# Kernel tuning notes

Hardware: AMD Instinct MI355X
Metric: run time of the kernel (lower is better)

The kernel has to match this reference:

```python
import jax, jax.numpy as jnp
import numpy as np

STEPS = 8
TOL = 1e-6


def _kabsch(p, q):
    # p, q: [B, N, 3]; returns R [B,3,3], t [B,3] s.t. q ~= R p + t (pypose svdtf)
    pm = p.mean(axis=-2, keepdims=True)
    qm = q.mean(axis=-2, keepdims=True)
    pc = p - pm
    qc = q - qm
    H = jnp.einsum('bni,bnj->bij', pc, qc)          # 3x3 cross-covariance
    U, S, Vt = jnp.linalg.svd(H, full_matrices=False)
    V = jnp.swapaxes(Vt, -1, -2)
    Ut = jnp.swapaxes(U, -1, -2)
    d = jnp.linalg.det(jnp.matmul(V, Ut))            # reflection fix
    D = jnp.concatenate([jnp.ones(d.shape + (2,), d.dtype), d[..., None]], axis=-1)
    R = jnp.matmul(V * D[..., None, :], Ut)
    t = qm[..., 0, :] - jnp.einsum('bij,bj->bi', R, pm[..., 0, :])
    return R, t


def _rotmat_to_quat(R):
    # branchless rotation-matrix -> quaternion [qx, qy, qz, qw] (pypose order)
    r00, r11, r22 = R[..., 0, 0], R[..., 1, 1], R[..., 2, 2]
    qw = 0.5 * jnp.sqrt(jnp.clip(1.0 + r00 + r11 + r22, 1e-12))
    qx = 0.5 * jnp.sqrt(jnp.clip(1.0 + r00 - r11 - r22, 1e-12))
    qy = 0.5 * jnp.sqrt(jnp.clip(1.0 - r00 + r11 - r22, 1e-12))
    qz = 0.5 * jnp.sqrt(jnp.clip(1.0 - r00 - r11 + r22, 1e-12))
    qx = qx * jnp.where(R[..., 2, 1] - R[..., 1, 2] >= 0, 1.0, -1.0)
    qy = qy * jnp.where(R[..., 0, 2] - R[..., 2, 0] >= 0, 1.0, -1.0)
    qz = qz * jnp.where(R[..., 1, 0] - R[..., 0, 1] >= 0, 1.0, -1.0)
    return jnp.stack([qx, qy, qz, qw], axis=-1)


def _icp(psrc, ptgt):
    B = psrc.shape[0]
    tn = (ptgt * ptgt).sum(-1)                        # [B, M]

    def body(carry, _):
        pc, err, done = carry
        # brute-force 1-NN: Euclidean cdist via  |p|^2 + |q|^2 - 2 p.q
        sq = ((pc * pc).sum(-1)[:, :, None] + tn[:, None, :]
              - 2.0 * jnp.einsum('bnd,bmd->bnm', pc, ptgt))
        dist = jnp.sqrt(jnp.clip(sq, 0.0))            # [B, N, M]
        knnd = dist.min(axis=-1)                      # [B, N]
        idx = dist.argmin(axis=-1)                    # [B, N]
        errnew = knnd.mean(axis=-1)                   # [B]
        conv = jnp.all(jnp.abs(errnew - err) < TOL)
        done_new = jnp.logical_or(done, conv)
        qk = jnp.take_along_axis(ptgt, jnp.broadcast_to(idx[..., None], pc.shape), axis=1)
        R, t = _kabsch(pc, qk)
        pcnew = jnp.einsum('bij,bnj->bni', R, pc) + t[:, None, :]
        pc = jnp.where(done_new, pc, pcnew)
        err = jnp.where(done_new, err, errnew)
        return (pc, err, done_new), None

    init = (psrc, jnp.zeros((B,), psrc.dtype), jnp.array(False))
    (pc, _, _), _ = jax.lax.scan(body, init, None, length=STEPS)
    R, t = _kabsch(psrc, pc)                          # final fit psrc -> moved cloud
    quat = _rotmat_to_quat(R)
    return jnp.concatenate([t, quat], axis=-1)        # SE3 7-vector [t, qx,qy,qz,qw]


def setup_inputs() -> dict:
    key = jax.random.key(0)
    k1, k2 = jax.random.split(key)
    psrc = jax.random.normal(k1, (2, 4096, 3), dtype=jnp.float32)
    ptgt = jax.random.normal(k2, (2, 4096, 3), dtype=jnp.float32)
    return {"psrc": psrc, "ptgt": ptgt}


def reference(psrc, ptgt):
    return _icp(psrc, ptgt)
```

## Files before the change

### kernel.cpp

```cpp
#include <hip/hip_runtime.h>
#include <math.h>

#define NPTS 4096
#define MPTS 4096
#define NSTEPS 8
#define ICP_TOL 1e-6f
#define NBLK 512
#define NSUB 32

#define ACC_OFF 32768
#define CTR_OFF 98304
#define CTR_STRIDE 1536
#define STPUB_OFF 110592

__global__ void init_kernel(const float* __restrict__ ptgt, float* __restrict__ ws) {
    float* ptgt4 = ws;
    unsigned* ctrs = (unsigned*)(ws + CTR_OFF);
    int gid = blockIdx.x * 256 + threadIdx.x;
    if (gid < 2 * MPTS) {
        float x = ptgt[3 * gid + 0];
        float y = ptgt[3 * gid + 1];
        float z = ptgt[3 * gid + 2];
        float4 v;
        v.x = x; v.y = y; v.z = z;
        v.w = 0.5f * (x * x + y * y + z * z);
        ((float4*)ptgt4)[gid] = v;
    }
    for (int i = gid; i < NSTEPS * CTR_STRIDE; i += 8192) ctrs[i] = 0u;
}

__device__ __forceinline__ float frcp(float x) {
#if __has_builtin(__builtin_amdgcn_rcpf)
    return __builtin_amdgcn_rcpf(x);
#else
    return 1.f / x;
#endif
}
__device__ __forceinline__ float frsq(float x) {
#if __has_builtin(__builtin_amdgcn_rsqf)
    return __builtin_amdgcn_rsqf(x);
#else
    return 1.f / sqrtf(x);
#endif
}

#define DET3(a,b,c,d,e,f,g,h,i) \
    ((a)*((e)*(i)-(f)*(h)) - (b)*((d)*(i)-(f)*(g)) + (c)*((d)*(h)-(e)*(g)))

__device__ __forceinline__ void horn_quat(const float N[4][4], float q[4]) {
    float s = 1e-30f;
#pragma unroll
    for (int i = 0; i < 4; ++i)
#pragma unroll
        for (int j = 0; j < 4; ++j) s = fmaxf(s, fabsf(N[i][j]));
    float inv = frcp(s);
    float A[4][4], B[4][4];
#pragma unroll
    for (int i = 0; i < 4; ++i)
#pragma unroll
        for (int j = 0; j < 4; ++j) A[i][j] = N[i][j] * inv;
#pragma unroll
    for (int i = 0; i < 4; ++i)
#pragma unroll
        for (int j = i; j < 4; ++j) {
            float v = A[i][0]*A[0][j] + A[i][1]*A[1][j] + A[i][2]*A[2][j] + A[i][3]*A[3][j];
            B[i][j] = v; B[j][i] = v;
        }
    float p1 = A[0][0]+A[1][1]+A[2][2]+A[3][3];
    float p2 = B[0][0]+B[1][1]+B[2][2]+B[3][3];
    float p3 = 0.f, p4 = 0.f;
#pragma unroll
    for (int i = 0; i < 4; ++i)
#pragma unroll
        for (int j = 0; j < 4; ++j) { p3 += A[i][j]*B[i][j]; p4 += B[i][j]*B[i][j]; }
    float e1 = p1;
    float e2 = 0.5f*(e1*p1 - p2);
    float e3 = (e2*p1 - e1*p2 + p3)*(1.f/3.f);
    float e4 = 0.25f*(e3*p1 - e2*p2 + e1*p3 - p4);
    float lam = -3e38f;
#pragma unroll
    for (int i = 0; i < 4; ++i) {
        float r = A[i][i];
#pragma unroll
        for (int j = 0; j < 4; ++j) if (j != i) r += fabsf(A[i][j]);
        lam = fmaxf(lam, r);
    }
#pragma unroll
    for (int it = 0; it < 12; ++it) {
        float pv = (((lam - e1)*lam + e2)*lam - e3)*lam + e4;
        float dv = ((4.f*lam - 3.f*e1)*lam + 2.f*e2)*lam - e3;
        lam -= pv * frcp(dv);
    }
    float M[4][4];
#pragma unroll
    for (int i = 0; i < 4; ++i)
#pragma unroll
        for (int j = 0; j < 4; ++j) M[i][j] = A[i][j] - ((i == j) ? lam : 0.f);
    float C0 = DET3(M[1][1],M[1][2],M[1][3], M[2][1],M[2][2],M[2][3], M[3][1],M[3][2],M[3][3]);
    float C1 = DET3(M[0][0],M[0][2],M[0][3], M[2][0],M[2][2],M[2][3], M[3][0],M[3][2],M[3][3]);
    float C2 = DET3(M[0][0],M[0][1],M[0][3], M[1][0],M[1][1],M[1][3], M[3][0],M[3][1],M[3][3]);
    float C3 = DET3(M[0][0],M[0][1],M[0][2], M[1][0],M[1][1],M[1][2], M[2][0],M[2][1],M[2][2]);
    int is = 0; float cb = fabsf(C0);
    if (fabsf(C1) > cb) { cb = fabsf(C1); is = 1; }
    if (fabsf(C2) > cb) { cb = fabsf(C2); is = 2; }
    if (fabsf(C3) > cb) { cb = fabsf(C3); is = 3; }
    float v0, v1, v2, v3;
#define ROWCOF(a,b,c) { \
    v0 =  DET3(M[a][1],M[a][2],M[a][3], M[b][1],M[b][2],M[b][3], M[c][1],M[c][2],M[c][3]); \
    v1 = -DET3(M[a][0],M[a][2],M[a][3], M[b][0],M[b][2],M[b][3], M[c][0],M[c][2],M[c][3]); \
    v2 =  DET3(M[a][0],M[a][1],M[a][3], M[b][0],M[b][1],M[b][3], M[c][0],M[c][1],M[c][3]); \
    v3 = -DET3(M[a][0],M[a][1],M[a][2], M[b][0],M[b][1],M[b][2], M[c][0],M[c][1],M[c][2]); }
    if (is == 0)      ROWCOF(1,2,3)
    else if (is == 1) ROWCOF(0,2,3)
    else if (is == 2) ROWCOF(0,1,3)
    else              ROWCOF(0,1,2)
#undef ROWCOF
    float nr = frsq(v0*v0 + v1*v1 + v2*v2 + v3*v3);
    q[0] = v0*nr; q[1] = v1*nr; q[2] = v2*nr; q[3] = v3*nr;
}

#define FOR16(OP) OP(0) OP(1) OP(2) OP(3) OP(4) OP(5) OP(6) OP(7) \
                  OP(8) OP(9) OP(10) OP(11) OP(12) OP(13) OP(14) OP(15)

__global__ __launch_bounds__(256, 2) void icp_main(
    const float* __restrict__ psrc, float* __restrict__ ws,
    float* __restrict__ out) {

    float* ptgt4 = ws;
    float* acc = ws + ACC_OFF;
    unsigned* ctrs = (unsigned*)(ws + CTR_OFF);
    float* stpub = ws + STPUB_OFF;

    __shared__ float st[2][13];
    __shared__ unsigned keys[4][16];
    __shared__ float red[16][16];
    __shared__ float gred[16][16];
    __shared__ float asum[2][16];
    __shared__ int contflag;

    const int tid = threadIdx.x;
    const int bid = blockIdx.x;
    const int b = bid >> 8;
    const int n0 = (bid & 255) * 16;

    if (tid < 2) {
        st[tid][0] = 1.f; st[tid][1] = 0.f; st[tid][2] = 0.f;
        st[tid][3] = 0.f; st[tid][4] = 1.f; st[tid][5] = 0.f;
        st[tid][6] = 0.f; st[tid][7] = 0.f; st[tid][8] = 1.f;
        st[tid][9] = 0.f; st[tid][10] = 0.f; st[tid][11] = 0.f;
        st[tid][12] = 0.f;
    }
    __syncthreads();

    const int w = tid >> 6, lane = tid & 63;
    const int m0 = w * 1024 + lane;
    const float4* tpb = (const float4*)ptgt4 + ((size_t)b * MPTS + m0);
    const float* ps = psrc + ((size_t)b * NPTS + n0) * 3;

    for (int step = 0; step < NSTEPS; ++step) {
        float R00 = st[b][0], R01 = st[b][1], R02 = st[b][2];
        float R10 = st[b][3], R11 = st[b][4], R12 = st[b][5];
        float R20 = st[b][6], R21 = st[b][7], R22 = st[b][8];
        float t0 = st[b][9], t1 = st[b][10], t2 = st[b][11];

#define DECLP(i) float px##i, py##i, pz##i;
        FOR16(DECLP)
#undef DECLP
#define LOADP(i) { float x = ps[3*(i)], y = ps[3*(i)+1], z = ps[3*(i)+2]; \
        px##i = fmaf(R00, x, fmaf(R01, y, fmaf(R02, z, t0))); \
        py##i = fmaf(R10, x, fmaf(R11, y, fmaf(R12, z, t1))); \
        pz##i = fmaf(R20, x, fmaf(R21, y, fmaf(R22, z, t2))); }
        FOR16(LOADP)
#undef LOADP

#define DECLB(i) float bs##i = -3.0e38f; int ix##i = m0;
        FOR16(DECLB)
#undef DECLB

        float4 tc0 = tpb[0];
        float4 tc1 = tpb[64];
        int mreg = m0;
#pragma unroll
        for (int k = 0; k < 16; ++k) {
            float4 tnx = tpb[((k + 2) & 15) * 64];
            float tx = tc0.x, ty = tc0.y, tz = tc0.z, htn = tc0.w;
#define PAIR(i) { float s = fmaf(px##i, tx, fmaf(py##i, ty, fmaf(pz##i, tz, -htn))); \
            if (s > bs##i) { bs##i = s; ix##i = mreg; } }
            FOR16(PAIR)
#undef PAIR
            mreg += 64;
            tc0 = tc1;
            tc1 = tnx;
        }

#define REDKEY(i) { unsigned ub = __float_as_uint(bs##i); \
        unsigned u = ((int)ub >= 0) ? (ub | 0x80000000u) : ~ub; \
        unsigned key = (u & 0xFFFFF000u) | (4095u - (unsigned)ix##i); \
        for (int off = 32; off; off >>= 1) { \
            unsigned o = (unsigned)__shfl_xor((int)key, off); \
            key = key > o ? key : o; } \
        if (lane == 0) keys[w][i] = key; }
        FOR16(REDKEY)
#undef REDKEY
        __syncthreads();

        if (tid < 16) {
            unsigned key = keys[0][tid];
            unsigned k1 = keys[1][tid], k2 = keys[2][tid], k3 = keys[3][tid];
            key = key > k1 ? key : k1;
            key = key > k2 ? key : k2;
            key = key > k3 ? key : k3;
            int m = 4095 - (int)(key & 0xFFFu);
            float4 qq = ((const float4*)ptgt4)[(size_t)b * MPTS + m];
            const float* pp = psrc + ((size_t)b * NPTS + n0 + tid) * 3;
            float x = pp[0], y = pp[1], z = pp[2];
            float px = fmaf(R00, x, fmaf(R01, y, fmaf(R02, z, t0)));
            float py = fmaf(R10, x, fmaf(R11, y, fmaf(R12, z, t1)));
            float pz = fmaf(R20, x, fmaf(R21, y, fmaf(R22, z, t2)));
            float dx = px - qq.x, dy = py - qq.y, dz = pz - qq.z;
            float dist = sqrtf(dx * dx + dy * dy + dz * dz);
            red[tid][0] = px; red[tid][1] = py; red[tid][2] = pz;
            red[tid][3] = qq.x; red[tid][4] = qq.y; red[tid][5] = qq.z;
            red[tid][6] = px * qq.x;  red[tid][7] = px * qq.y;  red[tid][8] = px * qq.z;
            red[tid][9] = py * qq.x;  red[tid][10] = py * qq.y; red[tid][11] = py * qq.z;
            red[tid][12] = pz * qq.x; red[tid][13] = pz * qq.y; red[tid][14] = pz * qq.z;
            red[tid][15] = dist;
        }
        __syncthreads();
        if (tid < 16) {
            float s = 0.f;
#pragma unroll
            for (int r = 0; r < 16; ++r) s += red[r][tid];
            __hip_atomic_store(&acc[((size_t)step * NBLK + bid) * 16 + tid], s,
                               __ATOMIC_RELAXED, __HIP_MEMORY_SCOPE_AGENT);
        }

        unsigned* stepc = ctrs + step * CTR_STRIDE;
        __syncthreads();
        if (tid == 0) {
            unsigned* sub = stepc + (bid & (NSUB - 1)) * 16;
            unsigned old = __hip_atomic_fetch_add(sub, 1u, __ATOMIC_RELAXED,
                                                  __HIP_MEMORY_SCOPE_AGENT);
            if (old == (unsigned)(NBLK / NSUB) - 1u)
                __hip_atomic_fetch_add(stepc + 512, 1u, __ATOMIC_RELAXED,
                                       __HIP_MEMORY_SCOPE_AGENT);
        }

        if (bid == 0) {
            if (tid == 0) {
                while (__hip_atomic_load(stepc + 512, __ATOMIC_RELAXED,
                                         __HIP_MEMORY_SCOPE_AGENT) < (unsigned)NSUB) {
                    __builtin_amdgcn_s_sleep(1);
                }
            }
            __syncthreads();
            {
                const float* accs = acc + (size_t)step * NBLK * 16;
                int c = tid & 15, g = tid >> 4;
                float ssum = 0.f;
#pragma unroll
                for (int i = 0; i < 32; ++i)
                    ssum += accs[(size_t)(g * 32 + i) * 16 + c];
                gred[g][c] = ssum;
            }
            __syncthreads();
            if (tid < 32) {
                int bb = tid >> 4, c = tid & 15;
                float s = 0.f;
#pragma unroll
                for (int g = 0; g < 8; ++g) s += gred[bb * 8 + g][c];
                asum[bb][c] = s;
            }
            __syncthreads();
            if (tid == 0) {
                float err0 = asum[0][15] * (1.f / NPTS);
                float err1 = asum[1][15] * (1.f / NPTS);
                bool conv = (fabsf(err0 - st[0][12]) < ICP_TOL) &&
                            (fabsf(err1 - st[1][12]) < ICP_TOL);
                contflag = conv ? 2 : 1;
            }
            __syncthreads();
            if (contflag == 1 && tid < 2) {
                float a[16];
                for (int i = 0; i < 16; ++i) a[i] = asum[tid][i];
                const float inv_n = 1.f / NPTS;
                float pmx = a[0]*inv_n, pmy = a[1]*inv_n, pmz = a[2]*inv_n;
                float qmx = a[3]*inv_n, qmy = a[4]*inv_n, qmz = a[5]*inv_n;
                float H[3][3];
                for (int i = 0; i < 3; ++i)
                    for (int j = 0; j < 3; ++j)
                        H[i][j] = a[6 + 3*i + j] - a[i]*a[3 + j]*inv_n;
                float Sxx=H[0][0], Sxy=H[0][1], Sxz=H[0][2];
                float Syx=H[1][0], Syy=H[1][1], Syz=H[1][2];
                float Szx=H[2][0], Szy=H[2][1], Szz=H[2][2];
                float Nm[4][4];
                Nm[0][0] = Sxx+Syy+Szz; Nm[0][1] = Syz-Szy;
                Nm[0][2] = Szx-Sxz;     Nm[0][3] = Sxy-Syx;
                Nm[1][1] = Sxx-Syy-Szz; Nm[1][2] = Sxy+Syx; Nm[1][3] = Szx+Sxz;
                Nm[2][2] = -Sxx+Syy-Szz; Nm[2][3] = Syz+Szy;
                Nm[3][3] = -Sxx-Syy+Szz;
                Nm[1][0]=Nm[0][1]; Nm[2][0]=Nm[0][2]; Nm[3][0]=Nm[0][3];
                Nm[2][1]=Nm[1][2]; Nm[3][1]=Nm[1][3]; Nm[3][2]=Nm[2][3];
                float qv[4];
                horn_quat(Nm, qv);
                float qw = qv[0], qx = qv[1], qy = qv[2], qz = qv[3];
                float R00n = 1.f - 2.f*(qy*qy + qz*qz);
                float R01n = 2.f*(qx*qy - qw*qz);
                float R02n = 2.f*(qx*qz + qw*qy);
                float R10n = 2.f*(qx*qy + qw*qz);
                float R11n = 1.f - 2.f*(qx*qx + qz*qz);
                float R12n = 2.f*(qy*qz - qw*qx);
                float R20n = 2.f*(qx*qz - qw*qy);
                float R21n = 2.f*(qy*qz + qw*qx);
                float R22n = 1.f - 2.f*(qx*qx + qy*qy);
                float tx = qmx - (R00n*pmx + R01n*pmy + R02n*pmz);
                float ty = qmy - (R10n*pmx + R11n*pmy + R12n*pmz);
                float tz = qmz - (R20n*pmx + R21n*pmy + R22n*pmz);
                float C00=st[tid][0], C01=st[tid][1], C02=st[tid][2];
                float C10=st[tid][3], C11=st[tid][4], C12=st[tid][5];
                float C20=st[tid][6], C21=st[tid][7], C22=st[tid][8];
                float T0=st[tid][9], T1=st[tid][10], T2=st[tid][11];
                float ns[12];
                ns[0] = R00n*C00 + R01n*C10 + R02n*C20;
                ns[1] = R00n*C01 + R01n*C11 + R02n*C21;
                ns[2] = R00n*C02 + R01n*C12 + R02n*C22;
                ns[3] = R10n*C00 + R11n*C10 + R12n*C20;
                ns[4] = R10n*C01 + R11n*C11 + R12n*C21;
                ns[5] = R10n*C02 + R11n*C12 + R12n*C22;
                ns[6] = R20n*C00 + R21n*C10 + R22n*C20;
                ns[7] = R20n*C01 + R21n*C11 + R22n*C21;
                ns[8] = R20n*C02 + R21n*C12 + R22n*C22;
                ns[9]  = R00n*T0 + R01n*T1 + R02n*T2 + tx;
                ns[10] = R10n*T0 + R11n*T1 + R12n*T2 + ty;
                ns[11] = R20n*T0 + R21n*T1 + R22n*T2 + tz;
                for (int i = 0; i < 12; ++i) {
                    st[tid][i] = ns[i];
                    __hip_atomic_store(&stpub[step*32 + tid*16 + i], ns[i],
                                       __ATOMIC_RELAXED, __HIP_MEMORY_SCOPE_AGENT);
                }
                st[tid][12] = asum[tid][15] * (1.f / NPTS);
            }
            __syncthreads();
            if (tid == 0) {
                unsigned fv = (unsigned)contflag;
#pragma unroll
                for (int f = 0; f < 32; ++f)
                    __hip_atomic_store(stepc + 1024 + f*16, fv,
                                       __ATOMIC_RELAXED, __HIP_MEMORY_SCOPE_AGENT);
            }
            __syncthreads();
        } else {
            if (tid == 0) {
                unsigned* myflag = stepc + 1024 + (bid & 31) * 16;
                unsigned fv;
                while ((fv = __hip_atomic_load(myflag, __ATOMIC_RELAXED,
                                               __HIP_MEMORY_SCOPE_AGENT)) == 0u) {
                    __builtin_amdgcn_s_sleep(2);
                }
                contflag = (int)fv;
                if (fv == 1u) {
                    for (int i = 0; i < 12; ++i)
                        st[b][i] = __hip_atomic_load(&stpub[step*32 + b*16 + i],
                                                     __ATOMIC_RELAXED,
                                                     __HIP_MEMORY_SCOPE_AGENT);
                }
            }
            __syncthreads();
        }
        if (contflag == 2) break;
    }

    if (bid == 0 && tid < 2) {
        float r00 = st[tid][0], r01 = st[tid][1], r02 = st[tid][2];
        float r10 = st[tid][3], r11 = st[tid][4], r12 = st[tid][5];
        float r20 = st[tid][6], r21 = st[tid][7], r22 = st[tid][8];
        float qw = 0.5f * sqrtf(fmaxf(1.f + r00 + r11 + r22, 1e-12f));
        float qx = 0.5f * sqrtf(fmaxf(1.f + r00 - r11 - r22, 1e-12f));
        float qy = 0.5f * sqrtf(fmaxf(1.f - r00 + r11 - r22, 1e-12f));
        float qz = 0.5f * sqrtf(fmaxf(1.f - r00 - r11 + r22, 1e-12f));
        qx = (r21 - r12 >= 0.f) ? qx : -qx;
        qy = (r02 - r20 >= 0.f) ? qy : -qy;
        qz = (r10 - r01 >= 0.f) ? qz : -qz;
        out[tid * 7 + 0] = st[tid][9];
        out[tid * 7 + 1] = st[tid][10];
        out[tid * 7 + 2] = st[tid][11];
        out[tid * 7 + 3] = qx;
        out[tid * 7 + 4] = qy;
        out[tid * 7 + 5] = qz;
        out[tid * 7 + 6] = qw;
    }
}

extern "C" void kernel_launch(void* const* d_in, const int* in_sizes, int n_in,
                              void* d_out, int out_size, void* d_ws, size_t ws_size,
                              hipStream_t stream) {
    const float* psrc = (const float*)d_in[0];
    const float* ptgt = (const float*)d_in[1];
    float* out = (float*)d_out;
    float* ws = (float*)d_ws;

    init_kernel<<<32, 256, 0, stream>>>(ptgt, ws);
    icp_main<<<NBLK, 256, 0, stream>>>(psrc, ws, out);
}
```

Before: 174.0 us.

## Replace master-block reduce-and-broadcast with redundant per-block reduction after grid barrier

Previously block 0 waited for all blocks, reduced the partial sums, ran the Horn solve and published the new transform, while every other block spun waiting for it. Now the last block to arrive at the hierarchical counter sets the release flags, and every block then reads all partial sums itself and runs the same reduction and solve locally. This removes one serialized publish-and-wait round trip per step, leaving a single barrier. The cost is 512 blocks each reading the full accumulator array (about 32 KB per step) and repeating the small solve, and all blocks must compute identical results for the convergence decision to stay consistent.

```diff
diff --git a/kernel.cpp b/kernel.cpp
--- a/kernel.cpp
+++ b/kernel.cpp
@@ -11,7 +11,6 @@
 #define ACC_OFF 32768
 #define CTR_OFF 98304
 #define CTR_STRIDE 1536
-#define STPUB_OFF 110592
 
 __global__ void init_kernel(const float* __restrict__ ptgt, float* __restrict__ ws) {
     float* ptgt4 = ws;
@@ -129,7 +128,6 @@
     float* ptgt4 = ws;
     float* acc = ws + ACC_OFF;
     unsigned* ctrs = (unsigned*)(ws + CTR_OFF);
-    float* stpub = ws + STPUB_OFF;
 
     __shared__ float st[2][13];
     __shared__ unsigned keys[4][16];
@@ -239,134 +237,114 @@
         __syncthreads();
         if (tid == 0) {
             unsigned* sub = stepc + (bid & (NSUB - 1)) * 16;
+            bool bcast = false;
             unsigned old = __hip_atomic_fetch_add(sub, 1u, __ATOMIC_RELAXED,
                                                   __HIP_MEMORY_SCOPE_AGENT);
-            if (old == (unsigned)(NBLK / NSUB) - 1u)
-                __hip_atomic_fetch_add(stepc + 512, 1u, __ATOMIC_RELAXED,
-                                       __HIP_MEMORY_SCOPE_AGENT);
-        }
-
-        if (bid == 0) {
-            if (tid == 0) {
-                while (__hip_atomic_load(stepc + 512, __ATOMIC_RELAXED,
-                                         __HIP_MEMORY_SCOPE_AGENT) < (unsigned)NSUB) {
+            if (old == (unsigned)(NBLK / NSUB) - 1u) {
+                unsigned mold = __hip_atomic_fetch_add(stepc + 512, 1u,
+                                    __ATOMIC_RELAXED, __HIP_MEMORY_SCOPE_AGENT);
+                if (mold == (unsigned)NSUB - 1u) {
+#pragma unroll
+                    for (int f = 0; f < NSUB; ++f)
+                        __hip_atomic_store(stepc + 1024 + f * 16, 1u,
+                                           __ATOMIC_RELAXED,
+                                           __HIP_MEMORY_SCOPE_AGENT);
+                    bcast = true;
+                }
+            }
+            if (!bcast) {
+                unsigned* myflag = stepc + 1024 + (bid & (NSUB - 1)) * 16;
+                while (__hip_atomic_load(myflag, __ATOMIC_RELAXED,
+                                         __HIP_MEMORY_SCOPE_AGENT) == 0u) {
                     __builtin_amdgcn_s_sleep(1);
                 }
             }
-            __syncthreads();
-            {
-                const float* accs = acc + (size_t)step * NBLK * 16;
-                int c = tid & 15, g = tid >> 4;
-                float ssum = 0.f;
-#pragma unroll
-                for (int i = 0; i < 32; ++i)
-                    ssum += accs[(size_t)(g * 32 + i) * 16 + c];
-                gred[g][c] = ssum;
-            }
-            __syncthreads();
-            if (tid < 32) {
-                int bb = tid >> 4, c = tid & 15;
-                float s = 0.f;
-#pragma unroll
-                for (int g = 0; g < 8; ++g) s += gred[bb * 8 + g][c];
-                asum[bb][c] = s;
-            }
-            __syncthreads();
-            if (tid == 0) {
-                float err0 = asum[0][15] * (1.f / NPTS);
-                float err1 = asum[1][15] * (1.f / NPTS);
-                bool conv = (fabsf(err0 - st[0][12]) < ICP_TOL) &&
-                            (fabsf(err1 - st[1][12]) < ICP_TOL);
-                contflag = conv ? 2 : 1;
-            }
-            __syncthreads();
-            if (contflag == 1 && tid < 2) {
-                float a[16];
-                for (int i = 0; i < 16; ++i) a[i] = asum[tid][i];
-                const float inv_n = 1.f / NPTS;
-                float pmx = a[0]*inv_n, pmy = a[1]*inv_n, pmz = a[2]*inv_n;
-                float qmx = a[3]*inv_n, qmy = a[4]*inv_n, qmz = a[5]*inv_n;
-                float H[3][3];
-                for (int i = 0; i < 3; ++i)
-                    for (int j = 0; j < 3; ++j)
-                        H[i][j] = a[6 + 3*i + j] - a[i]*a[3 + j]*inv_n;
-                float Sxx=H[0][0], Sxy=H[0][1], Sxz=H[0][2];
-                float Syx=H[1][0], Syy=H[1][1], Syz=H[1][2];
-                float Szx=H[2][0], Szy=H[2][1], Szz=H[2][2];
-                float Nm[4][4];
-                Nm[0][0] = Sxx+Syy+Szz; Nm[0][1] = Syz-Szy;
-                Nm[0][2] = Szx-Sxz;     Nm[0][3] = Sxy-Syx;
-                Nm[1][1] = Sxx-Syy-Szz; Nm[1][2] = Sxy+Syx; Nm[1][3] = Szx+Sxz;
-                Nm[2][2] = -Sxx+Syy-Szz; Nm[2][3] = Syz+Szy;
-                Nm[3][3] = -Sxx-Syy+Szz;
-                Nm[1][0]=Nm[0][1]; Nm[2][0]=Nm[0][2]; Nm[3][0]=Nm[0][3];
-                Nm[2][1]=Nm[1][2]; Nm[3][1]=Nm[1][3]; Nm[3][2]=Nm[2][3];
-                float qv[4];
-                horn_quat(Nm, qv);
-                float qw = qv[0], qx = qv[1], qy = qv[2], qz = qv[3];
-                float R00n = 1.f - 2.f*(qy*qy + qz*qz);
-                float R01n = 2.f*(qx*qy - qw*qz);
-                float R02n = 2.f*(qx*qz + qw*qy);
-                float R10n = 2.f*(qx*qy + qw*qz);
-                float R11n = 1.f - 2.f*(qx*qx + qz*qz);
-                float R12n = 2.f*(qy*qz - qw*qx);
-                float R20n = 2.f*(qx*qz - qw*qy);
-                float R21n = 2.f*(qy*qz + qw*qx);
-                float R22n = 1.f - 2.f*(qx*qx + qy*qy);
-                float tx = qmx - (R00n*pmx + R01n*pmy + R02n*pmz);
-                float ty = qmy - (R10n*pmx + R11n*pmy + R12n*pmz);
-                float tz = qmz - (R20n*pmx + R21n*pmy + R22n*pmz);
-                float C00=st[tid][0], C01=st[tid][1], C02=st[tid][2];
-                float C10=st[tid][3], C11=st[tid][4], C12=st[tid][5];
-                float C20=st[tid][6], C21=st[tid][7], C22=st[tid][8];
-                float T0=st[tid][9], T1=st[tid][10], T2=st[tid][11];
-                float ns[12];
-                ns[0] = R00n*C00 + R01n*C10 + R02n*C20;
-                ns[1] = R00n*C01 + R01n*C11 + R02n*C21;
-                ns[2] = R00n*C02 + R01n*C12 + R02n*C22;
-                ns[3] = R10n*C00 + R11n*C10 + R12n*C20;
-                ns[4] = R10n*C01 + R11n*C11 + R12n*C21;
-                ns[5] = R10n*C02 + R11n*C12 + R12n*C22;
-                ns[6] = R20n*C00 + R21n*C10 + R22n*C20;
-                ns[7] = R20n*C01 + R21n*C11 + R22n*C21;
-                ns[8] = R20n*C02 + R21n*C12 + R22n*C22;
-                ns[9]  = R00n*T0 + R01n*T1 + R02n*T2 + tx;
-                ns[10] = R10n*T0 + R11n*T1 + R12n*T2 + ty;
-                ns[11] = R20n*T0 + R21n*T1 + R22n*T2 + tz;
-                for (int i = 0; i < 12; ++i) {
-                    st[tid][i] = ns[i];
-                    __hip_atomic_store(&stpub[step*32 + tid*16 + i], ns[i],
-                                       __ATOMIC_RELAXED, __HIP_MEMORY_SCOPE_AGENT);
-                }
-                st[tid][12] = asum[tid][15] * (1.f / NPTS);
-            }
-            __syncthreads();
-            if (tid == 0) {
-                unsigned fv = (unsigned)contflag;
-#pragma unroll
-                for (int f = 0; f < 32; ++f)
-                    __hip_atomic_store(stepc + 1024 + f*16, fv,
-                                       __ATOMIC_RELAXED, __HIP_MEMORY_SCOPE_AGENT);
-            }
-            __syncthreads();
-        } else {
-            if (tid == 0) {
-                unsigned* myflag = stepc + 1024 + (bid & 31) * 16;
-                unsigned fv;
-                while ((fv = __hip_atomic_load(myflag, __ATOMIC_RELAXED,
-                                               __HIP_MEMORY_SCOPE_AGENT)) == 0u) {
-                    __builtin_amdgcn_s_sleep(2);
-                }
-                contflag = (int)fv;
-                if (fv == 1u) {
-                    for (int i = 0; i < 12; ++i)
-                        st[b][i] = __hip_atomic_load(&stpub[step*32 + b*16 + i],
-                                                     __ATOMIC_RELAXED,
-                                                     __HIP_MEMORY_SCOPE_AGENT);
-                }
-            }
-            __syncthreads();
-        }
+        }
+        __syncthreads();
+
+        {
+            const float* accs = acc + (size_t)step * NBLK * 16;
+            int c = tid & 15, g = tid >> 4;
+            float ssum = 0.f;
+#pragma unroll
+            for (int i = 0; i < 32; ++i)
+                ssum += accs[(size_t)(g * 32 + i) * 16 + c];
+            gred[g][c] = ssum;
+        }
+        __syncthreads();
+        if (tid < 32) {
+            int bb = tid >> 4, c = tid & 15;
+            float s = 0.f;
+#pragma unroll
+            for (int g = 0; g < 8; ++g) s += gred[bb * 8 + g][c];
+            asum[bb][c] = s;
+        }
+        __syncthreads();
+        if (tid == 0) {
+            float err0 = asum[0][15] * (1.f / NPTS);
+            float err1 = asum[1][15] * (1.f / NPTS);
+            bool conv = (fabsf(err0 - st[0][12]) < ICP_TOL) &&
+                        (fabsf(err1 - st[1][12]) < ICP_TOL);
+            contflag = conv ? 2 : 1;
+        }
+        __syncthreads();
+        if (contflag == 1 && tid < 2) {
+            float a[16];
+            for (int i = 0; i < 16; ++i) a[i] = asum[tid][i];
+            const float inv_n = 1.f / NPTS;
+            float pmx = a[0]*inv_n, pmy = a[1]*inv_n, pmz = a[2]*inv_n;
+            float qmx = a[3]*inv_n, qmy = a[4]*inv_n, qmz = a[5]*inv_n;
+            float H[3][3];
+            for (int i = 0; i < 3; ++i)
+                for (int j = 0; j < 3; ++j)
+                    H[i][j] = a[6 + 3*i + j] - a[i]*a[3 + j]*inv_n;
+            float Sxx=H[0][0], Sxy=H[0][1], Sxz=H[0][2];
+            float Syx=H[1][0], Syy=H[1][1], Syz=H[1][2];
+            float Szx=H[2][0], Szy=H[2][1], Szz=H[2][2];
+            float Nm[4][4];
+            Nm[0][0] = Sxx+Syy+Szz; Nm[0][1] = Syz-Szy;
+            Nm[0][2] = Szx-Sxz;     Nm[0][3] = Sxy-Syx;
+            Nm[1][1] = Sxx-Syy-Szz; Nm[1][2] = Sxy+Syx; Nm[1][3] = Szx+Sxz;
+            Nm[2][2] = -Sxx+Syy-Szz; Nm[2][3] = Syz+Szy;
+            Nm[3][3] = -Sxx-Syy+Szz;
+            Nm[1][0]=Nm[0][1]; Nm[2][0]=Nm[0][2]; Nm[3][0]=Nm[0][3];
+            Nm[2][1]=Nm[1][2]; Nm[3][1]=Nm[1][3]; Nm[3][2]=Nm[2][3];
+            float qv[4];
+            horn_quat(Nm, qv);
+            float qw = qv[0], qx = qv[1], qy = qv[2], qz = qv[3];
+            float R00n = 1.f - 2.f*(qy*qy + qz*qz);
+            float R01n = 2.f*(qx*qy - qw*qz);
+            float R02n = 2.f*(qx*qz + qw*qy);
+            float R10n = 2.f*(qx*qy + qw*qz);
+            float R11n = 1.f - 2.f*(qx*qx + qz*qz);
+            float R12n = 2.f*(qy*qz - qw*qx);
+            float R20n = 2.f*(qx*qz - qw*qy);
+            float R21n = 2.f*(qy*qz + qw*qx);
+            float R22n = 1.f - 2.f*(qx*qx + qy*qy);
+            float tx = qmx - (R00n*pmx + R01n*pmy + R02n*pmz);
+            float ty = qmy - (R10n*pmx + R11n*pmy + R12n*pmz);
+            float tz = qmz - (R20n*pmx + R21n*pmy + R22n*pmz);
+            float C00=st[tid][0], C01=st[tid][1], C02=st[tid][2];
+            float C10=st[tid][3], C11=st[tid][4], C12=st[tid][5];
+            float C20=st[tid][6], C21=st[tid][7], C22=st[tid][8];
+            float T0=st[tid][9], T1=st[tid][10], T2=st[tid][11];
+            float ns[12];
+            ns[0] = R00n*C00 + R01n*C10 + R02n*C20;
+            ns[1] = R00n*C01 + R01n*C11 + R02n*C21;
+            ns[2] = R00n*C02 + R01n*C12 + R02n*C22;
+            ns[3] = R10n*C00 + R11n*C10 + R12n*C20;
+            ns[4] = R10n*C01 + R11n*C11 + R12n*C21;
+            ns[5] = R10n*C02 + R11n*C12 + R12n*C22;
+            ns[6] = R20n*C00 + R21n*C10 + R22n*C20;
+            ns[7] = R20n*C01 + R21n*C11 + R22n*C21;
+            ns[8] = R20n*C02 + R21n*C12 + R22n*C22;
+            ns[9]  = R00n*T0 + R01n*T1 + R02n*T2 + tx;
+            ns[10] = R10n*T0 + R11n*T1 + R12n*T2 + ty;
+            ns[11] = R20n*T0 + R21n*T1 + R22n*T2 + tz;
+            for (int i = 0; i < 12; ++i) st[tid][i] = ns[i];
+            st[tid][12] = asum[tid][15] * (1.f / NPTS);
+        }
+        __syncthreads();
         if (contflag == 2) break;
     }
 
```

Measured after the change: 166.0 us. 4.6% less time.
